# Performance work log

Hardware: AMD Instinct MI355X
Metric: run time of the kernel (lower is better)

## Reference

```python
import jax, jax.numpy as jnp
import numpy as np

N_NODES = 50000
N_EDGES = 600000
HID = 128
OUT = 14
LAYERS = 3
N_GRAPHS = 16
NODE_VOCAB = (120, 6)
EDGE_VOCAB = (6, 3)
GEN_EPS = 1e-7   # GENConv eps added after ReLU on messages
BN_EPS = 1e-5    # torch BatchNorm1d default eps


def setup_inputs() -> dict:
    key = jax.random.key(0)
    ks = jax.random.split(key, 14)
    inp = {}
    inp['node_feat0'] = jax.random.randint(ks[0], (N_NODES,), 0, NODE_VOCAB[0], dtype=jnp.int32)
    inp['node_feat1'] = jax.random.randint(ks[1], (N_NODES,), 0, NODE_VOCAB[1], dtype=jnp.int32)
    inp['edge_feat0'] = jax.random.randint(ks[2], (N_EDGES,), 0, EDGE_VOCAB[0], dtype=jnp.int32)
    inp['edge_feat1'] = jax.random.randint(ks[3], (N_EDGES,), 0, EDGE_VOCAB[1], dtype=jnp.int32)
    inp['edge_src'] = jax.random.randint(ks[4], (N_EDGES,), 0, N_NODES, dtype=jnp.int32)
    inp['edge_dst'] = jax.random.randint(ks[5], (N_EDGES,), 0, N_NODES, dtype=jnp.int32)
    inp['graph_ids'] = jnp.repeat(jnp.arange(N_GRAPHS, dtype=jnp.int32), N_NODES // N_GRAPHS)
    inp['num_graphs'] = N_GRAPHS
    s = 0.05
    inp['W_node0'] = jax.random.normal(ks[6], (NODE_VOCAB[0], HID), jnp.float32) * s
    inp['W_node1'] = jax.random.normal(ks[7], (NODE_VOCAB[1], HID), jnp.float32) * s
    # per-layer edge embedding tables (each GENConv layer has its own)
    inp['edge_emb0'] = jax.random.normal(ks[8], (LAYERS, EDGE_VOCAB[0], HID), jnp.float32) * s
    inp['edge_emb1'] = jax.random.normal(ks[9], (LAYERS, EDGE_VOCAB[1], HID), jnp.float32) * s
    inp['beta'] = jnp.ones((LAYERS,), jnp.float32)  # learnable softmax temperature, init 1.0
    inp['mlp_W'] = jax.random.normal(ks[10], (LAYERS, HID, HID), jnp.float32) * (1.0 / np.sqrt(HID))
    inp['mlp_b'] = jnp.zeros((LAYERS, HID), jnp.float32)
    inp['bn_gamma'] = jnp.ones((LAYERS, HID), jnp.float32)
    inp['bn_beta'] = jnp.zeros((LAYERS, HID), jnp.float32)
    inp['W_out'] = jax.random.normal(ks[11], (HID, OUT), jnp.float32) * (1.0 / np.sqrt(HID))
    inp['b_out'] = jnp.zeros((OUT,), jnp.float32)
    return inp


def _segment_softmax(z, seg, num_segments):
    # DGL edge_softmax: elementwise softmax over edges sharing a destination node.
    zmax = jax.ops.segment_max(z, seg, num_segments=num_segments)
    zmax = jnp.where(jnp.isfinite(zmax), zmax, 0.0)  # guard empty segments
    e = jnp.exp(z - zmax[seg])
    denom = jax.ops.segment_sum(e, seg, num_segments=num_segments)
    return e / denom[seg]


def reference(node_feat0, node_feat1, edge_feat0, edge_feat1, edge_src, edge_dst,
              graph_ids, num_graphs, W_node0, W_node1, edge_emb0, edge_emb1,
              beta, mlp_W, mlp_b, bn_gamma, bn_beta, W_out, b_out):
    # node embedding lookup + sum over tables
    hv = W_node0[node_feat0] + W_node1[node_feat1]          # [N, H]
    n = hv.shape[0]
    for l in range(mlp_W.shape[0]):
        # BatchNorm1d (training mode: batch stats, biased variance) + ReLU
        mu = jnp.mean(hv, axis=0)
        var = jnp.var(hv, axis=0)
        hv1 = (hv - mu) * jax.lax.rsqrt(var + BN_EPS) * bn_gamma[l] + bn_beta[l]
        hv1 = jax.nn.relu(hv1)
        # GENConv: edge embed sum, u_add_e, relu+eps, edge_softmax, scatter-sum
        ee = edge_emb0[l][edge_feat0] + edge_emb1[l][edge_feat1]   # [E, H]
        m = jax.nn.relu(hv1[edge_src] + ee) + GEN_EPS              # [E, H]
        a = _segment_softmax(m * beta[l], edge_dst, n)             # [E, H]
        agg = jax.ops.segment_sum(m * a, edge_dst, num_segments=n)  # [N, H]
        # feats = node_feats + msg, then 1-layer MLP, then outer skip connect
        hv = (hv1 + agg) @ mlp_W[l] + mlp_b[l] + hv
    # AvgPooling over each graph in the batch, then output Linear
    counts = jax.ops.segment_sum(jnp.ones((n,), hv.dtype), graph_ids, num_segments=num_graphs)
    hg = jax.ops.segment_sum(hv, graph_ids, num_segments=num_graphs) / counts[:, None]
    return hg @ W_out + b_out  # [num_graphs, OUT]
```

## Files before the change

kernel.cpp:

```cpp
#include <hip/hip_runtime.h>

#define N_NODESC 50000
#define N_EDGESC 600000
#define HID 128
#define LAYERS 3
#define N_GRAPHSC 16
#define OUT_DIM 14
#define GEN_EPS 1e-7f
#define BN_EPS 1e-5f
#define SCAN_BLK 196
#define POOL_BLK 400
#define EMB_BLK 6250
#define GEMM_BLK 782
#define XPAD 50048
#define LOG2E 1.44269504f

typedef short bf16x8 __attribute__((ext_vector_type(8)));
typedef float f32x4 __attribute__((ext_vector_type(4)));

__device__ __forceinline__ unsigned short f2bf(float f) {
    union { float f; unsigned u; } v; v.f = f;
    unsigned r = v.u + 0x7FFF + ((v.u >> 16) & 1);
    return (unsigned short)(r >> 16);
}
__device__ __forceinline__ float bf_lo(unsigned u) {
    return __uint_as_float(u << 16);
}
__device__ __forceinline__ float bf_hi(unsigned u) {
    return __uint_as_float(u & 0xFFFF0000u);
}

__global__ void k_count(const int* __restrict__ dst, int* __restrict__ deg) {
    int i = blockIdx.x * blockDim.x + threadIdx.x;
    if (i < N_EDGESC) atomicAdd(&deg[dst[i]], 1);
}

__global__ void k_blocksum(const int* __restrict__ deg, int* __restrict__ part) {
    __shared__ int sh[256];
    int t = threadIdx.x;
    int i = blockIdx.x * 256 + t;
    sh[t] = (i < N_NODESC) ? deg[i] : 0;
    __syncthreads();
    for (int off = 128; off > 0; off >>= 1) {
        if (t < off) sh[t] += sh[t + off];
        __syncthreads();
    }
    if (t == 0) part[blockIdx.x] = sh[0];
}

__global__ void k_scanpart(const int* __restrict__ part, int* __restrict__ bofs) {
    __shared__ int sh[256];
    int t = threadIdx.x;
    int v = (t < SCAN_BLK) ? part[t] : 0;
    sh[t] = v;
    __syncthreads();
    for (int off = 1; off < 256; off <<= 1) {
        int add = (t >= off) ? sh[t - off] : 0;
        __syncthreads();
        sh[t] += add;
        __syncthreads();
    }
    if (t < SCAN_BLK) bofs[t] = sh[t] - v;
}

__global__ void k_rowptr(const int* __restrict__ deg, const int* __restrict__ bofs,
                         int* __restrict__ row_ptr, int* __restrict__ cursor) {
    __shared__ int sh[256];
    int t = threadIdx.x;
    int i = blockIdx.x * 256 + t;
    int d = (i < N_NODESC) ? deg[i] : 0;
    sh[t] = d;
    __syncthreads();
    for (int off = 1; off < 256; off <<= 1) {
        int add = (t >= off) ? sh[t - off] : 0;
        __syncthreads();
        sh[t] += add;
        __syncthreads();
    }
    if (i < N_NODESC) {
        int rp = bofs[blockIdx.x] + sh[t] - d;
        row_ptr[i] = rp;
        cursor[i] = rp;
    }
    if (i == 0) row_ptr[N_NODESC] = N_EDGESC;
}

__global__ void k_scatter(const int* __restrict__ dst, const int* __restrict__ src,
                          const int* __restrict__ f0, const int* __restrict__ f1,
                          int* __restrict__ cursor, int* __restrict__ csr_pack) {
    int i = blockIdx.x * blockDim.x + threadIdx.x;
    if (i < N_EDGESC) {
        int pos = atomicAdd(&cursor[dst[i]], 1);
        csr_pack[pos] = (src[i] << 8) | ((f0[i] * 3 + f1[i]) * 8);
    }
}

__global__ void k_wfrag(const float* __restrict__ W, unsigned short* __restrict__ wf) {
    int i = blockIdx.x * blockDim.x + threadIdx.x;
    if (i >= LAYERS * 4 * 8 * 64 * 8) return;
    int j = i & 7;
    int lane = (i >> 3) & 63;
    int nt = (i >> 9) & 7;
    int ks = (i >> 12) & 3;
    int l = i >> 14;
    int k = ks * 32 + (lane >> 4) * 8 + j;
    int n = nt * 16 + (lane & 15);
    wf[i] = f2bf(W[(size_t)l * HID * HID + k * HID + n]);
}

__global__ void k_embed(const int* __restrict__ f0, const int* __restrict__ f1,
                        const float4* __restrict__ W0, const float4* __restrict__ W1,
                        float4* __restrict__ hv4, float* __restrict__ part) {
    __shared__ float sh[1024], sh2[1024];
    int tid = threadIdx.x;
    int i = blockIdx.x * 256 + tid;
    int v = i >> 5, c4 = i & 31;
    float4 a = W0[f0[v] * 32 + c4];
    float4 b = W1[f1[v] * 32 + c4];
    float4 o = make_float4(a.x + b.x, a.y + b.y, a.z + b.z, a.w + b.w);
    hv4[i] = o;
    sh[tid * 4 + 0] = o.x; sh2[tid * 4 + 0] = o.x * o.x;
    sh[tid * 4 + 1] = o.y; sh2[tid * 4 + 1] = o.y * o.y;
    sh[tid * 4 + 2] = o.z; sh2[tid * 4 + 2] = o.z * o.z;
    sh[tid * 4 + 3] = o.w; sh2[tid * 4 + 3] = o.w * o.w;
    __syncthreads();
    if (tid < 128) {
        int c4i = tid >> 2, j = tid & 3;
        float s = 0.f, s2 = 0.f;
#pragma unroll
        for (int r = 0; r < 8; r++) {
            s += sh[(r * 32 + c4i) * 4 + j];
            s2 += sh2[(r * 32 + c4i) * 4 + j];
        }
        part[(size_t)blockIdx.x * 256 + tid] = s;
        part[(size_t)blockIdx.x * 256 + 128 + tid] = s2;
    }
}

__global__ void k_bn_reduce2(const float* __restrict__ part, int nparts,
                             float* __restrict__ gsum) {
    int slot = blockIdx.x;
    int t = threadIdx.x;
    float s = 0.f;
    for (int p = t; p < nparts; p += 256) s += part[(size_t)p * 256 + slot];
    __shared__ float sh[256];
    sh[t] = s;
    __syncthreads();
    for (int o = 128; o > 0; o >>= 1) {
        if (t < o) sh[t] += sh[t + o];
        __syncthreads();
    }
    if (t == 0) gsum[slot] = sh[0];
}

__global__ void k_hv1b(const float4* __restrict__ hv4, const float* __restrict__ gsum,
                       const float* __restrict__ gamma, const float* __restrict__ betab,
                       uint2* __restrict__ hv1b) {
    int i = blockIdx.x * 256 + threadIdx.x;
    int c = (i & 31) * 4;
    const float invN = 1.f / (float)N_NODESC;
    float4 h = hv4[i];
    float r[4];
#pragma unroll
    for (int j = 0; j < 4; j++) {
        float mu = gsum[c + j] * invN;
        float var = gsum[128 + c + j] * invN - mu * mu;
        float sc = gamma[c + j] * rsqrtf(var + BN_EPS);
        float sf = betab[c + j] - mu * sc;
        r[j] = fmaxf(fmaf((&h.x)[j], sc, sf), 0.f);
    }
    uint2 o;
    o.x = (unsigned)f2bf(r[0]) | ((unsigned)f2bf(r[1]) << 16);
    o.y = (unsigned)f2bf(r[2]) | ((unsigned)f2bf(r[3]) << 16);
    hv1b[i] = o;
}

__global__ __launch_bounds__(512) void k_agg(
    const unsigned* __restrict__ hv1b, const int* __restrict__ row_ptr,
    const int* __restrict__ csr_pack, const float* __restrict__ e0,
    const float* __restrict__ e1, const float* __restrict__ beta_p,
    unsigned* __restrict__ xb) {
    __shared__ float2 sh_et[64][19];
    int tid = threadIdx.x;
    for (int i = tid; i < 18 * 64; i += 512) {
        int f = i >> 6, ln = i & 63;
        int a = f / 3, b = f - 3 * a;
        float2 ea = *(const float2*)(e0 + a * HID + 2 * ln);
        float2 eb = *(const float2*)(e1 + b * HID + 2 * ln);
        sh_et[ln][f] = make_float2(ea.x + eb.x, ea.y + eb.y);
    }
    int wave = tid >> 6, lane = tid & 63;
    int v = blockIdx.x * 8 + wave;
    float beta = *beta_p;
    const float bl2 = beta * LOG2E;
    __syncthreads();
    unsigned su = hv1b[(size_t)v * 64 + lane];
    float h10 = bf_lo(su), h11 = bf_hi(su);
    int p0 = row_ptr[v], p1 = row_ptr[v + 1];
    int deg = p1 - p0;
    float n0 = 0.f, n1 = 0.f, d0 = 0.f, d1 = 0.f;
    const char* hv1c = (const char*)hv1b;
    const char* etc = (const char*)&sh_et[lane][0];
    unsigned lane4 = (unsigned)lane * 4;

#define AGG_BODY(J)                                                         \
    {                                                                       \
        int pack = __shfl(pk, (J), 64);                                     \
        unsigned u = *(const unsigned*)(hv1c +                              \
                        ((((unsigned)pack) & 0xFFFFFF00u) + lane4));        \
        float2 t = *(const float2*)(etc + (((unsigned)pack) & 0xFFu));      \
        float r0 = fmaxf(bf_lo(u) + t.x, 0.f);                              \
        float r1 = fmaxf(bf_hi(u) + t.y, 0.f);                              \
        float w0 = exp2f(r0 * bl2);                                         \
        float w1 = exp2f(r1 * bl2);                                         \
        d0 += w0; d1 += w1;                                                 \
        n0 = fmaf(r0, w0, n0); n1 = fmaf(r1, w1, n1);                       \
    }

    for (int base = 0; base < deg; base += 64) {
        int idx = base + lane;
        int pk = (idx < deg) ? csr_pack[p0 + idx] : 0;
        int jn = min(64, deg - base);
        int j = 0;
        for (; j + 2 <= jn; j += 2) {
            AGG_BODY(j)
            AGG_BODY(j + 1)
        }
        if (j < jn) AGG_BODY(j)
    }
#undef AGG_BODY

    float ox = h10 + (deg ? __fdividef(n0, d0) + GEN_EPS : 0.f);
    float oy = h11 + (deg ? __fdividef(n1, d1) + GEN_EPS : 0.f);
    xb[(size_t)v * 64 + lane] = (unsigned)f2bf(ox) | ((unsigned)f2bf(oy) << 16);
}

__global__ __launch_bounds__(256) void k_gemm(
    const unsigned short* __restrict__ x,
    const unsigned short* __restrict__ wf,
    const float* __restrict__ b, float* __restrict__ hv,
    float* __restrict__ part) {
    __shared__ float shs[512], shs2[512];
    int tid = threadIdx.x;
    int w = tid >> 6, lane = tid & 63;
    int m0 = blockIdx.x * 64 + w * 16;
    int mrow = lane & 15, grp = lane >> 4;
    bf16x8 af[4];
    const unsigned short* xrow = x + (size_t)(m0 + mrow) * HID + grp * 8;
#pragma unroll
    for (int ks = 0; ks < 4; ks++)
        af[ks] = *(const bf16x8*)(xrow + ks * 32);
    f32x4 acc[8];
#pragma unroll
    for (int nt = 0; nt < 8; nt++) acc[nt] = (f32x4){0.f, 0.f, 0.f, 0.f};
#pragma unroll
    for (int nt = 0; nt < 8; nt++) {
#pragma unroll
        for (int ks = 0; ks < 4; ks++) {
            bf16x8 bf = *(const bf16x8*)(wf + (size_t)((ks * 8 + nt) * 64 + lane) * 8);
            acc[nt] = __builtin_amdgcn_mfma_f32_16x16x32_bf16(af[ks], bf, acc[nt], 0, 0, 0);
        }
    }
#pragma unroll
    for (int nt = 0; nt < 8; nt++) {
        int col = nt * 16 + mrow;
        float bias = b[col];
        float s = 0.f, s2 = 0.f;
#pragma unroll
        for (int r = 0; r < 4; r++) {
            int v = m0 + grp * 4 + r;
            if (v < N_NODESC) {
                size_t idx = (size_t)v * HID + col;
                float o = acc[nt][r] + bias + hv[idx];
                hv[idx] = o;
                s += o; s2 += o * o;
            }
        }
        s  += __shfl_xor(s, 16, 64);  s  += __shfl_xor(s, 32, 64);
        s2 += __shfl_xor(s2, 16, 64); s2 += __shfl_xor(s2, 32, 64);
        if (lane < 16) { shs[w * 128 + col] = s; shs2[w * 128 + col] = s2; }
    }
    __syncthreads();
    if (tid < 128) {
        part[(size_t)blockIdx.x * 256 + tid] =
            shs[tid] + shs[128 + tid] + shs[256 + tid] + shs[384 + tid];
    } else {
        int c = tid - 128;
        part[(size_t)blockIdx.x * 256 + tid] =
            shs2[c] + shs2[128 + c] + shs2[256 + c] + shs2[384 + c];
    }
}

__global__ void k_pool(const float* __restrict__ hv, float* __restrict__ part2) {
    int tid = threadIdx.x;
    int c = tid & 127, rh = tid >> 7;
    int start = blockIdx.x * 125;
    float acc = 0.f;
    for (int r = start + rh; r < start + 125; r += 2)
        acc += hv[(size_t)r * HID + c];
    __shared__ float sh[256];
    sh[tid] = acc;
    __syncthreads();
    if (rh == 0) part2[blockIdx.x * 128 + c] = acc + sh[tid + 128];
}

__global__ void k_finish(const float* __restrict__ part2, const float* __restrict__ Wo,
                         const float* __restrict__ bo, float* __restrict__ out) {
    __shared__ float hg[N_GRAPHSC * HID];
    int t = threadIdx.x;
    for (int s = t; s < N_GRAPHSC * HID; s += 256) {
        int g = s >> 7, c = s & 127;
        float x = 0.f;
#pragma unroll
        for (int i = 0; i < 25; i++) x += part2[(g * 25 + i) * 128 + c];
        hg[s] = x;
    }
    __syncthreads();
    if (t < N_GRAPHSC * OUT_DIM) {
        int g = t / OUT_DIM, o = t % OUT_DIM;
        const float inv = (float)N_GRAPHSC / (float)N_NODESC;
        float acc = bo[o];
        for (int k = 0; k < HID; k++)
            acc += hg[g * HID + k] * inv * Wo[k * OUT_DIM + o];
        out[t] = acc;
    }
}

extern "C" void kernel_launch(void* const* d_in, const int* in_sizes, int n_in,
                              void* d_out, int out_size, void* d_ws, size_t ws_size,
                              hipStream_t stream) {
    const int* node_feat0 = (const int*)d_in[0];
    const int* node_feat1 = (const int*)d_in[1];
    const int* edge_feat0 = (const int*)d_in[2];
    const int* edge_feat1 = (const int*)d_in[3];
    const int* edge_src   = (const int*)d_in[4];
    const int* edge_dst   = (const int*)d_in[5];
    const float* W_node0   = (const float*)d_in[8];
    const float* W_node1   = (const float*)d_in[9];
    const float* edge_emb0 = (const float*)d_in[10];
    const float* edge_emb1 = (const float*)d_in[11];
    const float* beta      = (const float*)d_in[12];
    const float* mlp_W     = (const float*)d_in[13];
    const float* mlp_b     = (const float*)d_in[14];
    const float* bn_gamma  = (const float*)d_in[15];
    const float* bn_beta   = (const float*)d_in[16];
    const float* W_out     = (const float*)d_in[17];
    const float* b_out     = (const float*)d_in[18];
    float* out = (float*)d_out;

    char* ws = (char*)d_ws;
    size_t off = 0;
    auto alloc = [&](size_t bytes) -> void* {
        void* p = ws + off;
        off += (bytes + 255) & ~(size_t)255;
        return p;
    };
    float* hv      = (float*)alloc((size_t)N_NODESC * HID * 4);
    unsigned* xb   = (unsigned*)alloc((size_t)XPAD * 64 * 4);
    unsigned* hv1b = (unsigned*)alloc((size_t)N_NODESC * 64 * 4);
    float* bnpart  = (float*)alloc((size_t)EMB_BLK * 256 * 4);
    float* gsum    = (float*)alloc(256 * 4);
    unsigned short* wfrag = (unsigned short*)alloc((size_t)LAYERS * 16384 * 2);
    float* part2   = (float*)alloc(POOL_BLK * 128 * 4);
    int* row_ptr   = (int*)alloc((N_NODESC + 1) * 4);
    int* cursor    = (int*)alloc(N_NODESC * 4);
    int* deg       = (int*)alloc(N_NODESC * 4);
    int* part      = (int*)alloc(SCAN_BLK * 4);
    int* bofs      = (int*)alloc(SCAN_BLK * 4);
    int* csr_pack  = (int*)alloc((size_t)N_EDGESC * 4);

    hipMemsetAsync(deg, 0, N_NODESC * 4, stream);
    k_count<<<(N_EDGESC + 255) / 256, 256, 0, stream>>>(edge_dst, deg);
    k_blocksum<<<SCAN_BLK, 256, 0, stream>>>(deg, part);
    k_scanpart<<<1, 256, 0, stream>>>(part, bofs);
    k_rowptr<<<SCAN_BLK, 256, 0, stream>>>(deg, bofs, row_ptr, cursor);
    k_scatter<<<(N_EDGESC + 255) / 256, 256, 0, stream>>>(
        edge_dst, edge_src, edge_feat0, edge_feat1, cursor, csr_pack);
    k_wfrag<<<(LAYERS * 16384 + 255) / 256, 256, 0, stream>>>(mlp_W, wfrag);

    k_embed<<<EMB_BLK, 256, 0, stream>>>(
        node_feat0, node_feat1, (const float4*)W_node0, (const float4*)W_node1,
        (float4*)hv, bnpart);

    for (int l = 0; l < LAYERS; l++) {
        int nparts = (l == 0) ? EMB_BLK : GEMM_BLK;
        k_bn_reduce2<<<256, 256, 0, stream>>>(bnpart, nparts, gsum);
        k_hv1b<<<(N_NODESC * 32) / 256, 256, 0, stream>>>(
            (const float4*)hv, gsum, bn_gamma + l * HID, bn_beta + l * HID,
            (uint2*)hv1b);
        k_agg<<<N_NODESC / 8, 512, 0, stream>>>(
            hv1b, row_ptr, csr_pack,
            edge_emb0 + (size_t)l * 6 * HID, edge_emb1 + (size_t)l * 3 * HID,
            beta + l, xb);
        k_gemm<<<GEMM_BLK, 256, 0, stream>>>(
            (const unsigned short*)xb, wfrag + (size_t)l * 16384,
            mlp_b + l * HID, hv, bnpart);
    }

    k_pool<<<POOL_BLK, 256, 0, stream>>>(hv, part2);
    k_finish<<<1, 256, 0, stream>>>(part2, W_out, b_out, out);
}
```

Baseline: 454.9 us.

## Process two edges per wave in aggregation with wider loads; atomic BN reduce

The aggregation kernel now has each half-wave handle a different edge, with each lane loading 4 bf16 features (8 bytes) and a float4 edge-embedding entry, so two edges are processed per iteration. The half-wave partial sums are combined with a cross-half shuffle at the end. An odd trailing edge is masked for the second half. The BN statistics reduction switches from 256 blocks with a strided column gather to 64 blocks with coalesced row sums combined via atomicAdd into per-layer zeroed buffers. This reduces instruction count per edge and improves coalescing, but atomics make the reduction order nondeterministic.

```diff
diff --git a/kernel.cpp b/kernel.cpp
--- a/kernel.cpp
+++ b/kernel.cpp
@@ -13,6 +13,7 @@
 #define EMB_BLK 6250
 #define GEMM_BLK 782
 #define XPAD 50048
+#define BNR_BLK 64
 #define LOG2E 1.44269504f
 
 typedef short bf16x8 __attribute__((ext_vector_type(8)));
@@ -139,18 +140,13 @@
 
 __global__ void k_bn_reduce2(const float* __restrict__ part, int nparts,
                              float* __restrict__ gsum) {
-    int slot = blockIdx.x;
     int t = threadIdx.x;
+    int rows = (nparts + BNR_BLK - 1) / BNR_BLK;
+    int r0 = blockIdx.x * rows;
+    int r1 = min(r0 + rows, nparts);
     float s = 0.f;
-    for (int p = t; p < nparts; p += 256) s += part[(size_t)p * 256 + slot];
-    __shared__ float sh[256];
-    sh[t] = s;
-    __syncthreads();
-    for (int o = 128; o > 0; o >>= 1) {
-        if (t < o) sh[t] += sh[t + o];
-        __syncthreads();
-    }
-    if (t == 0) gsum[slot] = sh[0];
+    for (int p = r0; p < r1; p++) s += part[(size_t)p * 256 + t];
+    atomicAdd(&gsum[t], s);
 }
 
 __global__ void k_hv1b(const float4* __restrict__ hv4, const float* __restrict__ gsum,
@@ -180,59 +176,95 @@
     const int* __restrict__ csr_pack, const float* __restrict__ e0,
     const float* __restrict__ e1, const float* __restrict__ beta_p,
     unsigned* __restrict__ xb) {
-    __shared__ float2 sh_et[64][19];
+    __shared__ float4 sh_et[18 * 32];
     int tid = threadIdx.x;
-    for (int i = tid; i < 18 * 64; i += 512) {
-        int f = i >> 6, ln = i & 63;
+    for (int i = tid; i < 18 * 32; i += 512) {
+        int f = i >> 5, s = i & 31;
         int a = f / 3, b = f - 3 * a;
-        float2 ea = *(const float2*)(e0 + a * HID + 2 * ln);
-        float2 eb = *(const float2*)(e1 + b * HID + 2 * ln);
-        sh_et[ln][f] = make_float2(ea.x + eb.x, ea.y + eb.y);
+        float4 ea = *(const float4*)(e0 + a * HID + 4 * s);
+        float4 eb = *(const float4*)(e1 + b * HID + 4 * s);
+        sh_et[i] = make_float4(ea.x + eb.x, ea.y + eb.y, ea.z + eb.z, ea.w + eb.w);
     }
     int wave = tid >> 6, lane = tid & 63;
+    int h = lane >> 5, s = lane & 31;
     int v = blockIdx.x * 8 + wave;
     float beta = *beta_p;
     const float bl2 = beta * LOG2E;
-    __syncthreads();
-    unsigned su = hv1b[(size_t)v * 64 + lane];
-    float h10 = bf_lo(su), h11 = bf_hi(su);
+    const float hm = h ? 0.f : 1.f;
+    __syncthreads();
+    uint2 su = ((const uint2*)hv1b)[v * 32 + s];
     int p0 = row_ptr[v], p1 = row_ptr[v + 1];
     int deg = p1 - p0;
-    float n0 = 0.f, n1 = 0.f, d0 = 0.f, d1 = 0.f;
+    float n0 = 0.f, n1 = 0.f, n2 = 0.f, n3 = 0.f;
+    float d0 = 0.f, d1 = 0.f, d2 = 0.f, d3 = 0.f;
     const char* hv1c = (const char*)hv1b;
-    const char* etc = (const char*)&sh_et[lane][0];
-    unsigned lane4 = (unsigned)lane * 4;
-
-#define AGG_BODY(J)                                                         \
+    const char* etc = (const char*)sh_et;
+    unsigned s8 = (unsigned)s * 8;
+    unsigned s16 = (unsigned)s * 16;
+
+#define PAIR(J)                                                             \
     {                                                                       \
-        int pack = __shfl(pk, (J), 64);                                     \
-        unsigned u = *(const unsigned*)(hv1c +                              \
-                        ((((unsigned)pack) & 0xFFFFFF00u) + lane4));        \
-        float2 t = *(const float2*)(etc + (((unsigned)pack) & 0xFFu));      \
-        float r0 = fmaxf(bf_lo(u) + t.x, 0.f);                              \
-        float r1 = fmaxf(bf_hi(u) + t.y, 0.f);                              \
-        float w0 = exp2f(r0 * bl2);                                         \
-        float w1 = exp2f(r1 * bl2);                                         \
-        d0 += w0; d1 += w1;                                                 \
+        int pack = __shfl(pk, 2 * (J) + h, 64);                             \
+        uint2 u = *(const uint2*)(hv1c +                                    \
+                      ((((unsigned)pack) & 0xFFFFFF00u) | s8));             \
+        float4 t = *(const float4*)(etc +                                   \
+                      ((((unsigned)pack & 0xFFu) << 6) | s16));             \
+        float r0 = fmaxf(bf_lo(u.x) + t.x, 0.f);                            \
+        float r1 = fmaxf(bf_hi(u.x) + t.y, 0.f);                            \
+        float r2 = fmaxf(bf_lo(u.y) + t.z, 0.f);                            \
+        float r3 = fmaxf(bf_hi(u.y) + t.w, 0.f);                            \
+        float w0 = exp2f(r0 * bl2), w1 = exp2f(r1 * bl2);                   \
+        float w2 = exp2f(r2 * bl2), w3 = exp2f(r3 * bl2);                   \
+        d0 += w0; d1 += w1; d2 += w2; d3 += w3;                             \
         n0 = fmaf(r0, w0, n0); n1 = fmaf(r1, w1, n1);                       \
+        n2 = fmaf(r2, w2, n2); n3 = fmaf(r3, w3, n3);                       \
     }
 
     for (int base = 0; base < deg; base += 64) {
         int idx = base + lane;
         int pk = (idx < deg) ? csr_pack[p0 + idx] : 0;
         int jn = min(64, deg - base);
+        int pairs = jn >> 1;
         int j = 0;
-        for (; j + 2 <= jn; j += 2) {
-            AGG_BODY(j)
-            AGG_BODY(j + 1)
+        for (; j + 2 <= pairs; j += 2) {
+            PAIR(j)
+            PAIR(j + 1)
         }
-        if (j < jn) AGG_BODY(j)
-    }
-#undef AGG_BODY
-
-    float ox = h10 + (deg ? __fdividef(n0, d0) + GEN_EPS : 0.f);
-    float oy = h11 + (deg ? __fdividef(n1, d1) + GEN_EPS : 0.f);
-    xb[(size_t)v * 64 + lane] = (unsigned)f2bf(ox) | ((unsigned)f2bf(oy) << 16);
+        if (j < pairs) PAIR(j)
+        if (jn & 1) {
+            int pack = __shfl(pk, jn - 1, 64);
+            uint2 u = *(const uint2*)(hv1c +
+                          ((((unsigned)pack) & 0xFFFFFF00u) | s8));
+            float4 t = *(const float4*)(etc +
+                          ((((unsigned)pack & 0xFFu) << 6) | s16));
+            float r0 = fmaxf(bf_lo(u.x) + t.x, 0.f);
+            float r1 = fmaxf(bf_hi(u.x) + t.y, 0.f);
+            float r2 = fmaxf(bf_lo(u.y) + t.z, 0.f);
+            float r3 = fmaxf(bf_hi(u.y) + t.w, 0.f);
+            float w0 = exp2f(r0 * bl2) * hm, w1 = exp2f(r1 * bl2) * hm;
+            float w2 = exp2f(r2 * bl2) * hm, w3 = exp2f(r3 * bl2) * hm;
+            d0 += w0; d1 += w1; d2 += w2; d3 += w3;
+            n0 = fmaf(r0, w0, n0); n1 = fmaf(r1, w1, n1);
+            n2 = fmaf(r2, w2, n2); n3 = fmaf(r3, w3, n3);
+        }
+    }
+#undef PAIR
+
+    n0 += __shfl_xor(n0, 32, 64); d0 += __shfl_xor(d0, 32, 64);
+    n1 += __shfl_xor(n1, 32, 64); d1 += __shfl_xor(d1, 32, 64);
+    n2 += __shfl_xor(n2, 32, 64); d2 += __shfl_xor(d2, 32, 64);
+    n3 += __shfl_xor(n3, 32, 64); d3 += __shfl_xor(d3, 32, 64);
+
+    float o0 = bf_lo(su.x) + (deg ? __fdividef(n0, d0) + GEN_EPS : 0.f);
+    float o1 = bf_hi(su.x) + (deg ? __fdividef(n1, d1) + GEN_EPS : 0.f);
+    float o2 = bf_lo(su.y) + (deg ? __fdividef(n2, d2) + GEN_EPS : 0.f);
+    float o3 = bf_hi(su.y) + (deg ? __fdividef(n3, d3) + GEN_EPS : 0.f);
+    if (h == 0) {
+        uint2 ov;
+        ov.x = (unsigned)f2bf(o0) | ((unsigned)f2bf(o1) << 16);
+        ov.y = (unsigned)f2bf(o2) | ((unsigned)f2bf(o3) << 16);
+        ((uint2*)xb)[v * 32 + s] = ov;
+    }
 }
 
 __global__ __launch_bounds__(256) void k_gemm(
@@ -359,7 +391,7 @@
     unsigned* xb   = (unsigned*)alloc((size_t)XPAD * 64 * 4);
     unsigned* hv1b = (unsigned*)alloc((size_t)N_NODESC * 64 * 4);
     float* bnpart  = (float*)alloc((size_t)EMB_BLK * 256 * 4);
-    float* gsum    = (float*)alloc(256 * 4);
+    float* gsums   = (float*)alloc(LAYERS * 256 * 4);
     unsigned short* wfrag = (unsigned short*)alloc((size_t)LAYERS * 16384 * 2);
     float* part2   = (float*)alloc(POOL_BLK * 128 * 4);
     int* row_ptr   = (int*)alloc((N_NODESC + 1) * 4);
@@ -370,6 +402,7 @@
     int* csr_pack  = (int*)alloc((size_t)N_EDGESC * 4);
 
     hipMemsetAsync(deg, 0, N_NODESC * 4, stream);
+    hipMemsetAsync(gsums, 0, LAYERS * 256 * 4, stream);
     k_count<<<(N_EDGESC + 255) / 256, 256, 0, stream>>>(edge_dst, deg);
     k_blocksum<<<SCAN_BLK, 256, 0, stream>>>(deg, part);
     k_scanpart<<<1, 256, 0, stream>>>(part, bofs);
@@ -383,8 +416,9 @@
         (float4*)hv, bnpart);
 
     for (int l = 0; l < LAYERS; l++) {
+        float* gsum = gsums + l * 256;
         int nparts = (l == 0) ? EMB_BLK : GEMM_BLK;
-        k_bn_reduce2<<<256, 256, 0, stream>>>(bnpart, nparts, gsum);
+        k_bn_reduce2<<<BNR_BLK, 256, 0, stream>>>(bnpart, nparts, gsum);
         k_hv1b<<<(N_NODESC * 32) / 256, 256, 0, stream>>>(
             (const float4*)hv, gsum, bn_gamma + l * HID, bn_beta + l * HID,
             (uint2*)hv1b);
```

Measured after the change: 458.9 us. About the same (+0.9%).

## Split node features into 16-channel planes so gather working set fits cache

Applied to the files above, without the earlier changes.

Node features (hv1 and the aggregation output) are stored as 8 planes of 16 bf16 channels each instead of row-major 128 channels. Each aggregation block handles one plane for 64 nodes, with 8 lanes per node, so a gather touches a 1.6MB plane that can stay cache-resident instead of striding across the full feature matrix. The GEMM loads its A fragments from the planar layout. The BN-stat reduction now splits rows across 64 blocks and combines them with atomics into per-layer zeroed buffers. The cost is that each edge index is read 8 times (once per plane) and nodes in the same wave loop to the largest degree with masked work.

```diff
diff --git a/kernel.cpp b/kernel.cpp
--- a/kernel.cpp
+++ b/kernel.cpp
@@ -12,7 +12,11 @@
 #define POOL_BLK 400
 #define EMB_BLK 6250
 #define GEMM_BLK 782
-#define XPAD 50048
+#define BNR_BLK 64
+#define PLN 50048
+#define PLNW (PLN * 8)
+#define PLNS (PLN * 16)
+#define NCHUNK 8
 #define LOG2E 1.44269504f
 
 typedef short bf16x8 __attribute__((ext_vector_type(8)));
@@ -139,25 +143,21 @@
 
 __global__ void k_bn_reduce2(const float* __restrict__ part, int nparts,
                              float* __restrict__ gsum) {
-    int slot = blockIdx.x;
     int t = threadIdx.x;
+    int rows = (nparts + BNR_BLK - 1) / BNR_BLK;
+    int r0 = blockIdx.x * rows;
+    int r1 = min(r0 + rows, nparts);
     float s = 0.f;
-    for (int p = t; p < nparts; p += 256) s += part[(size_t)p * 256 + slot];
-    __shared__ float sh[256];
-    sh[t] = s;
-    __syncthreads();
-    for (int o = 128; o > 0; o >>= 1) {
-        if (t < o) sh[t] += sh[t + o];
-        __syncthreads();
-    }
-    if (t == 0) gsum[slot] = sh[0];
+    for (int p = r0; p < r1; p++) s += part[(size_t)p * 256 + t];
+    atomicAdd(&gsum[t], s);
 }
 
 __global__ void k_hv1b(const float4* __restrict__ hv4, const float* __restrict__ gsum,
                        const float* __restrict__ gamma, const float* __restrict__ betab,
-                       uint2* __restrict__ hv1b) {
+                       unsigned* __restrict__ hv1p) {
     int i = blockIdx.x * 256 + threadIdx.x;
-    int c = (i & 31) * 4;
+    int v = i >> 5, c4 = i & 31;
+    int c = c4 * 4;
     const float invN = 1.f / (float)N_NODESC;
     float4 h = hv4[i];
     float r[4];
@@ -172,67 +172,70 @@
     uint2 o;
     o.x = (unsigned)f2bf(r[0]) | ((unsigned)f2bf(r[1]) << 16);
     o.y = (unsigned)f2bf(r[2]) | ((unsigned)f2bf(r[3]) << 16);
-    hv1b[i] = o;
+    int ck = c4 >> 2;
+    *(uint2*)(hv1p + (size_t)ck * PLNW + (size_t)v * 8 + (c4 & 3) * 2) = o;
 }
 
 __global__ __launch_bounds__(512) void k_agg(
-    const unsigned* __restrict__ hv1b, const int* __restrict__ row_ptr,
+    const unsigned* __restrict__ hv1p, const int* __restrict__ row_ptr,
     const int* __restrict__ csr_pack, const float* __restrict__ e0,
     const float* __restrict__ e1, const float* __restrict__ beta_p,
-    unsigned* __restrict__ xb) {
-    __shared__ float2 sh_et[64][19];
+    unsigned* __restrict__ xbp) {
+    __shared__ float2 sh_et[18 * 8];
     int tid = threadIdx.x;
-    for (int i = tid; i < 18 * 64; i += 512) {
-        int f = i >> 6, ln = i & 63;
+    int ck = blockIdx.x & 7;
+    int ng = blockIdx.x >> 3;
+    if (tid < 144) {
+        int f = tid >> 3, sl = tid & 7;
         int a = f / 3, b = f - 3 * a;
-        float2 ea = *(const float2*)(e0 + a * HID + 2 * ln);
-        float2 eb = *(const float2*)(e1 + b * HID + 2 * ln);
-        sh_et[ln][f] = make_float2(ea.x + eb.x, ea.y + eb.y);
+        int c0 = ck * 16 + sl * 2;
+        float2 ea = *(const float2*)(e0 + a * HID + c0);
+        float2 eb = *(const float2*)(e1 + b * HID + c0);
+        sh_et[tid] = make_float2(ea.x + eb.x, ea.y + eb.y);
     }
     int wave = tid >> 6, lane = tid & 63;
-    int v = blockIdx.x * 8 + wave;
+    int oct = lane >> 3, s = lane & 7;
+    int v = ng * 64 + wave * 8 + oct;
     float beta = *beta_p;
     const float bl2 = beta * LOG2E;
     __syncthreads();
-    unsigned su = hv1b[(size_t)v * 64 + lane];
-    float h10 = bf_lo(su), h11 = bf_hi(su);
-    int p0 = row_ptr[v], p1 = row_ptr[v + 1];
-    int deg = p1 - p0;
+    const unsigned* plane = hv1p + (size_t)ck * PLNW;
+    unsigned su = plane[v * 8 + s];
+    int vc = min(v, N_NODESC);
+    int p0 = row_ptr[vc];
+    int deg = row_ptr[min(vc + 1, N_NODESC)] - p0;
+    int dd = deg;
+    dd = max(dd, __shfl_xor(dd, 8, 64));
+    dd = max(dd, __shfl_xor(dd, 16, 64));
+    dd = max(dd, __shfl_xor(dd, 32, 64));
+    int dmax = __builtin_amdgcn_readfirstlane(dd);
     float n0 = 0.f, n1 = 0.f, d0 = 0.f, d1 = 0.f;
-    const char* hv1c = (const char*)hv1b;
-    const char* etc = (const char*)&sh_et[lane][0];
-    unsigned lane4 = (unsigned)lane * 4;
-
-#define AGG_BODY(J)                                                         \
-    {                                                                       \
-        int pack = __shfl(pk, (J), 64);                                     \
-        unsigned u = *(const unsigned*)(hv1c +                              \
-                        ((((unsigned)pack) & 0xFFFFFF00u) + lane4));        \
-        float2 t = *(const float2*)(etc + (((unsigned)pack) & 0xFFu));      \
-        float r0 = fmaxf(bf_lo(u) + t.x, 0.f);                              \
-        float r1 = fmaxf(bf_hi(u) + t.y, 0.f);                              \
-        float w0 = exp2f(r0 * bl2);                                         \
-        float w1 = exp2f(r1 * bl2);                                         \
-        d0 += w0; d1 += w1;                                                 \
-        n0 = fmaf(r0, w0, n0); n1 = fmaf(r1, w1, n1);                       \
-    }
-
-    for (int base = 0; base < deg; base += 64) {
-        int idx = base + lane;
-        int pk = (idx < deg) ? csr_pack[p0 + idx] : 0;
-        int jn = min(64, deg - base);
-        int j = 0;
-        for (; j + 2 <= jn; j += 2) {
-            AGG_BODY(j)
-            AGG_BODY(j + 1)
-        }
-        if (j < jn) AGG_BODY(j)
-    }
-#undef AGG_BODY
-
-    float ox = h10 + (deg ? __fdividef(n0, d0) + GEN_EPS : 0.f);
-    float oy = h11 + (deg ? __fdividef(n1, d1) + GEN_EPS : 0.f);
-    xb[(size_t)v * 64 + lane] = (unsigned)f2bf(ox) | ((unsigned)f2bf(oy) << 16);
+    const char* pc = (const char*)plane;
+    const char* etc = (const char*)sh_et;
+    unsigned s4 = (unsigned)s * 4, s8 = (unsigned)s * 8;
+    int dm1 = deg - 1;
+#pragma unroll 2
+    for (int j = 0; j < dmax; j++) {
+        bool on = j < deg;
+        int pidx = min(p0 + max(0, min(j, dm1)), N_EDGESC - 1);
+        int pk = __builtin_nontemporal_load(&csr_pack[pidx]);
+        unsigned u = *(const unsigned*)(pc +
+                        ((((unsigned)pk & 0xFFFFFF00u) >> 3) | s4));
+        float2 t = *(const float2*)(etc +
+                        ((((unsigned)pk & 0xFFu) << 3) | s8));
+        float r0 = fmaxf(bf_lo(u) + t.x, 0.f);
+        float r1 = fmaxf(bf_hi(u) + t.y, 0.f);
+        float w0 = exp2f(r0 * bl2), w1 = exp2f(r1 * bl2);
+        w0 = on ? w0 : 0.f;
+        w1 = on ? w1 : 0.f;
+        d0 += w0; d1 += w1;
+        n0 = fmaf(r0, w0, n0); n1 = fmaf(r1, w1, n1);
+    }
+    float o0 = bf_lo(su) + (deg ? __fdividef(n0, d0) + GEN_EPS : 0.f);
+    float o1 = bf_hi(su) + (deg ? __fdividef(n1, d1) + GEN_EPS : 0.f);
+    if (v < N_NODESC)
+        xbp[(size_t)ck * PLNW + (size_t)v * 8 + s] =
+            (unsigned)f2bf(o0) | ((unsigned)f2bf(o1) << 16);
 }
 
 __global__ __launch_bounds__(256) void k_gemm(
@@ -246,10 +249,12 @@
     int m0 = blockIdx.x * 64 + w * 16;
     int mrow = lane & 15, grp = lane >> 4;
     bf16x8 af[4];
-    const unsigned short* xrow = x + (size_t)(m0 + mrow) * HID + grp * 8;
-#pragma unroll
-    for (int ks = 0; ks < 4; ks++)
-        af[ks] = *(const bf16x8*)(xrow + ks * 32);
+#pragma unroll
+    for (int ks = 0; ks < 4; ks++) {
+        int ckp = ks * 2 + (grp >> 1);
+        af[ks] = *(const bf16x8*)(x + (size_t)ckp * PLNS +
+                                  (size_t)(m0 + mrow) * 16 + (grp & 1) * 8);
+    }
     f32x4 acc[8];
 #pragma unroll
     for (int nt = 0; nt < 8; nt++) acc[nt] = (f32x4){0.f, 0.f, 0.f, 0.f};
@@ -356,10 +361,10 @@
         return p;
     };
     float* hv      = (float*)alloc((size_t)N_NODESC * HID * 4);
-    unsigned* xb   = (unsigned*)alloc((size_t)XPAD * 64 * 4);
-    unsigned* hv1b = (unsigned*)alloc((size_t)N_NODESC * 64 * 4);
+    unsigned* xbp  = (unsigned*)alloc((size_t)NCHUNK * PLNW * 4);
+    unsigned* hv1p = (unsigned*)alloc((size_t)NCHUNK * PLNW * 4);
     float* bnpart  = (float*)alloc((size_t)EMB_BLK * 256 * 4);
-    float* gsum    = (float*)alloc(256 * 4);
+    float* gsums   = (float*)alloc(LAYERS * 256 * 4);
     unsigned short* wfrag = (unsigned short*)alloc((size_t)LAYERS * 16384 * 2);
     float* part2   = (float*)alloc(POOL_BLK * 128 * 4);
     int* row_ptr   = (int*)alloc((N_NODESC + 1) * 4);
@@ -370,6 +375,7 @@
     int* csr_pack  = (int*)alloc((size_t)N_EDGESC * 4);
 
     hipMemsetAsync(deg, 0, N_NODESC * 4, stream);
+    hipMemsetAsync(gsums, 0, LAYERS * 256 * 4, stream);
     k_count<<<(N_EDGESC + 255) / 256, 256, 0, stream>>>(edge_dst, deg);
     k_blocksum<<<SCAN_BLK, 256, 0, stream>>>(deg, part);
     k_scanpart<<<1, 256, 0, stream>>>(part, bofs);
@@ -383,17 +389,17 @@
         (float4*)hv, bnpart);
 
     for (int l = 0; l < LAYERS; l++) {
+        float* gsum = gsums + l * 256;
         int nparts = (l == 0) ? EMB_BLK : GEMM_BLK;
-        k_bn_reduce2<<<256, 256, 0, stream>>>(bnpart, nparts, gsum);
+        k_bn_reduce2<<<BNR_BLK, 256, 0, stream>>>(bnpart, nparts, gsum);
         k_hv1b<<<(N_NODESC * 32) / 256, 256, 0, stream>>>(
-            (const float4*)hv, gsum, bn_gamma + l * HID, bn_beta + l * HID,
-            (uint2*)hv1b);
-        k_agg<<<N_NODESC / 8, 512, 0, stream>>>(
-            hv1b, row_ptr, csr_pack,
+            (const float4*)hv, gsum, bn_gamma + l * HID, bn_beta + l * HID, hv1p);
+        k_agg<<<GEMM_BLK * NCHUNK, 512, 0, stream>>>(
+            hv1p, row_ptr, csr_pack,
             edge_emb0 + (size_t)l * 6 * HID, edge_emb1 + (size_t)l * 3 * HID,
-            beta + l, xb);
+            beta + l, xbp);
         k_gemm<<<GEMM_BLK, 256, 0, stream>>>(
-            (const unsigned short*)xb, wfrag + (size_t)l * 16384,
+            (const unsigned short*)xbp, wfrag + (size_t)l * 16384,
             mlp_b + l * HID, hv, bnpart);
     }
 
```

After: 570.0 us. 25.3% more time.

## Fuse aggregation with MFMA GEMM via shared-memory tile, merge weight prep into embed

Applied to the files above, without the earlier changes.

Aggregation and the MLP GEMM become one kernel. Each 512-thread block aggregates 64 nodes into a swizzled LDS bf16 tile and then runs the MFMA GEMM from that tile, which removes the xb global round trip and one launch per layer. The weight-fragment conversion is folded into extra blocks of the embed kernel. The BN partial reduction now uses 64 blocks that atomically add into per-layer zeroed sums. In exchange, each wave now processes 8 nodes serially, which lowers grid parallelism in the latency-bound gather, and the float atomics make the sums order-nondeterministic.

```diff
diff --git a/kernel.cpp b/kernel.cpp
--- a/kernel.cpp
+++ b/kernel.cpp
@@ -11,8 +11,9 @@
 #define SCAN_BLK 196
 #define POOL_BLK 400
 #define EMB_BLK 6250
+#define WF_BLK 192
 #define GEMM_BLK 782
-#define XPAD 50048
+#define BNR_BLK 64
 #define LOG2E 1.44269504f
 
 typedef short bf16x8 __attribute__((ext_vector_type(8)));
@@ -95,24 +96,26 @@
     }
 }
 
-__global__ void k_wfrag(const float* __restrict__ W, unsigned short* __restrict__ wf) {
-    int i = blockIdx.x * blockDim.x + threadIdx.x;
-    if (i >= LAYERS * 4 * 8 * 64 * 8) return;
-    int j = i & 7;
-    int lane = (i >> 3) & 63;
-    int nt = (i >> 9) & 7;
-    int ks = (i >> 12) & 3;
-    int l = i >> 14;
-    int k = ks * 32 + (lane >> 4) * 8 + j;
-    int n = nt * 16 + (lane & 15);
-    wf[i] = f2bf(W[(size_t)l * HID * HID + k * HID + n]);
-}
-
 __global__ void k_embed(const int* __restrict__ f0, const int* __restrict__ f1,
                         const float4* __restrict__ W0, const float4* __restrict__ W1,
-                        float4* __restrict__ hv4, float* __restrict__ part) {
+                        float4* __restrict__ hv4, float* __restrict__ part,
+                        const float* __restrict__ W, unsigned short* __restrict__ wf) {
+    int tid = threadIdx.x;
+    if (blockIdx.x >= EMB_BLK) {
+        int i = (blockIdx.x - EMB_BLK) * 256 + tid;
+        if (i < LAYERS * 4 * 8 * 64 * 8) {
+            int j = i & 7;
+            int lane = (i >> 3) & 63;
+            int nt = (i >> 9) & 7;
+            int ks = (i >> 12) & 3;
+            int l = i >> 14;
+            int k = ks * 32 + (lane >> 4) * 8 + j;
+            int n = nt * 16 + (lane & 15);
+            wf[i] = f2bf(W[(size_t)l * HID * HID + k * HID + n]);
+        }
+        return;
+    }
     __shared__ float sh[1024], sh2[1024];
-    int tid = threadIdx.x;
     int i = blockIdx.x * 256 + tid;
     int v = i >> 5, c4 = i & 31;
     float4 a = W0[f0[v] * 32 + c4];
@@ -139,18 +142,13 @@
 
 __global__ void k_bn_reduce2(const float* __restrict__ part, int nparts,
                              float* __restrict__ gsum) {
-    int slot = blockIdx.x;
     int t = threadIdx.x;
+    int rows = (nparts + BNR_BLK - 1) / BNR_BLK;
+    int r0 = blockIdx.x * rows;
+    int r1 = min(r0 + rows, nparts);
     float s = 0.f;
-    for (int p = t; p < nparts; p += 256) s += part[(size_t)p * 256 + slot];
-    __shared__ float sh[256];
-    sh[t] = s;
-    __syncthreads();
-    for (int o = 128; o > 0; o >>= 1) {
-        if (t < o) sh[t] += sh[t + o];
-        __syncthreads();
-    }
-    if (t == 0) gsum[slot] = sh[0];
+    for (int p = r0; p < r1; p++) s += part[(size_t)p * 256 + t];
+    atomicAdd(&gsum[t], s);
 }
 
 __global__ void k_hv1b(const float4* __restrict__ hv4, const float* __restrict__ gsum,
@@ -175,40 +173,41 @@
     hv1b[i] = o;
 }
 
-__global__ __launch_bounds__(512) void k_agg(
+__global__ __launch_bounds__(512) void k_aggemm(
     const unsigned* __restrict__ hv1b, const int* __restrict__ row_ptr,
     const int* __restrict__ csr_pack, const float* __restrict__ e0,
     const float* __restrict__ e1, const float* __restrict__ beta_p,
-    unsigned* __restrict__ xb) {
-    __shared__ float2 sh_et[64][19];
+    const unsigned short* __restrict__ wf, const float* __restrict__ b,
+    float* __restrict__ hv, float* __restrict__ part) {
+    __shared__ float2 sh_et[18 * 64];
+    __shared__ unsigned x_tile[64 * 64];
+    __shared__ float shs[512], shs2[512];
     int tid = threadIdx.x;
     for (int i = tid; i < 18 * 64; i += 512) {
         int f = i >> 6, ln = i & 63;
-        int a = f / 3, b = f - 3 * a;
+        int a = f / 3, bb = f - 3 * a;
         float2 ea = *(const float2*)(e0 + a * HID + 2 * ln);
-        float2 eb = *(const float2*)(e1 + b * HID + 2 * ln);
-        sh_et[ln][f] = make_float2(ea.x + eb.x, ea.y + eb.y);
-    }
-    int wave = tid >> 6, lane = tid & 63;
-    int v = blockIdx.x * 8 + wave;
+        float2 eb = *(const float2*)(e1 + bb * HID + 2 * ln);
+        sh_et[i] = make_float2(ea.x + eb.x, ea.y + eb.y);
+    }
+    int w = tid >> 6, lane = tid & 63;
+    int m0 = blockIdx.x * 64;
     float beta = *beta_p;
     const float bl2 = beta * LOG2E;
     __syncthreads();
-    unsigned su = hv1b[(size_t)v * 64 + lane];
-    float h10 = bf_lo(su), h11 = bf_hi(su);
-    int p0 = row_ptr[v], p1 = row_ptr[v + 1];
-    int deg = p1 - p0;
-    float n0 = 0.f, n1 = 0.f, d0 = 0.f, d1 = 0.f;
+
     const char* hv1c = (const char*)hv1b;
-    const char* etc = (const char*)&sh_et[lane][0];
+    const char* etc = (const char*)sh_et;
     unsigned lane4 = (unsigned)lane * 4;
+    unsigned lane8 = (unsigned)lane * 8;
 
 #define AGG_BODY(J)                                                         \
     {                                                                       \
         int pack = __shfl(pk, (J), 64);                                     \
         unsigned u = *(const unsigned*)(hv1c +                              \
                         ((((unsigned)pack) & 0xFFFFFF00u) + lane4));        \
-        float2 t = *(const float2*)(etc + (((unsigned)pack) & 0xFFu));      \
+        float2 t = *(const float2*)(etc +                                   \
+                        (((((unsigned)pack) & 0xFFu) << 6) + lane8));       \
         float r0 = fmaxf(bf_lo(u) + t.x, 0.f);                              \
         float r1 = fmaxf(bf_hi(u) + t.y, 0.f);                              \
         float w0 = exp2f(r0 * bl2);                                         \
@@ -217,58 +216,63 @@
         n0 = fmaf(r0, w0, n0); n1 = fmaf(r1, w1, n1);                       \
     }
 
-    for (int base = 0; base < deg; base += 64) {
-        int idx = base + lane;
-        int pk = (idx < deg) ? csr_pack[p0 + idx] : 0;
-        int jn = min(64, deg - base);
-        int j = 0;
-        for (; j + 2 <= jn; j += 2) {
-            AGG_BODY(j)
-            AGG_BODY(j + 1)
+    for (int i = 0; i < 8; i++) {
+        int row = w * 8 + i;
+        int v = m0 + row;
+        int vc = min(v, N_NODESC - 1);
+        unsigned su = hv1b[(size_t)vc * 64 + lane];
+        int p0 = row_ptr[vc];
+        int deg = (v < N_NODESC) ? (row_ptr[vc + 1] - p0) : 0;
+        float n0 = 0.f, n1 = 0.f, d0 = 0.f, d1 = 0.f;
+        for (int base = 0; base < deg; base += 64) {
+            int idx = base + lane;
+            int pk = (idx < deg) ? csr_pack[p0 + idx] : 0;
+            int jn = min(64, deg - base);
+            int j = 0;
+            for (; j + 2 <= jn; j += 2) {
+                AGG_BODY(j)
+                AGG_BODY(j + 1)
+            }
+            if (j < jn) AGG_BODY(j)
         }
-        if (j < jn) AGG_BODY(j)
+        float ox = bf_lo(su) + (deg ? __fdividef(n0, d0) + GEN_EPS : 0.f);
+        float oy = bf_hi(su) + (deg ? __fdividef(n1, d1) + GEN_EPS : 0.f);
+        x_tile[row * 64 + ((lane + row * 4) & 63)] =
+            (unsigned)f2bf(ox) | ((unsigned)f2bf(oy) << 16);
     }
 #undef AGG_BODY
-
-    float ox = h10 + (deg ? __fdividef(n0, d0) + GEN_EPS : 0.f);
-    float oy = h11 + (deg ? __fdividef(n1, d1) + GEN_EPS : 0.f);
-    xb[(size_t)v * 64 + lane] = (unsigned)f2bf(ox) | ((unsigned)f2bf(oy) << 16);
-}
-
-__global__ __launch_bounds__(256) void k_gemm(
-    const unsigned short* __restrict__ x,
-    const unsigned short* __restrict__ wf,
-    const float* __restrict__ b, float* __restrict__ hv,
-    float* __restrict__ part) {
-    __shared__ float shs[512], shs2[512];
-    int tid = threadIdx.x;
-    int w = tid >> 6, lane = tid & 63;
-    int m0 = blockIdx.x * 64 + w * 16;
+    __syncthreads();
+
+    int rw = w & 3, chh = w >> 2;
     int mrow = lane & 15, grp = lane >> 4;
+    int rbase = rw * 16 + mrow;
     bf16x8 af[4];
-    const unsigned short* xrow = x + (size_t)(m0 + mrow) * HID + grp * 8;
-#pragma unroll
-    for (int ks = 0; ks < 4; ks++)
-        af[ks] = *(const bf16x8*)(xrow + ks * 32);
-    f32x4 acc[8];
-#pragma unroll
-    for (int nt = 0; nt < 8; nt++) acc[nt] = (f32x4){0.f, 0.f, 0.f, 0.f};
-#pragma unroll
-    for (int nt = 0; nt < 8; nt++) {
+#pragma unroll
+    for (int ks = 0; ks < 4; ks++) {
+        int col = ks * 16 + grp * 4;
+        int colr = (col + rbase * 4) & 63;
+        af[ks] = *(const bf16x8*)&x_tile[rbase * 64 + colr];
+    }
+    f32x4 acc[4];
+#pragma unroll
+    for (int nt = 0; nt < 4; nt++) acc[nt] = (f32x4){0.f, 0.f, 0.f, 0.f};
+#pragma unroll
+    for (int nt = 0; nt < 4; nt++) {
+        int ntg = chh * 4 + nt;
 #pragma unroll
         for (int ks = 0; ks < 4; ks++) {
-            bf16x8 bf = *(const bf16x8*)(wf + (size_t)((ks * 8 + nt) * 64 + lane) * 8);
-            acc[nt] = __builtin_amdgcn_mfma_f32_16x16x32_bf16(af[ks], bf, acc[nt], 0, 0, 0);
+            bf16x8 bfr = *(const bf16x8*)(wf + (size_t)((ks * 8 + ntg) * 64 + lane) * 8);
+            acc[nt] = __builtin_amdgcn_mfma_f32_16x16x32_bf16(af[ks], bfr, acc[nt], 0, 0, 0);
         }
     }
 #pragma unroll
-    for (int nt = 0; nt < 8; nt++) {
-        int col = nt * 16 + mrow;
+    for (int nt = 0; nt < 4; nt++) {
+        int col = chh * 64 + nt * 16 + mrow;
         float bias = b[col];
         float s = 0.f, s2 = 0.f;
 #pragma unroll
         for (int r = 0; r < 4; r++) {
-            int v = m0 + grp * 4 + r;
+            int v = m0 + rw * 16 + grp * 4 + r;
             if (v < N_NODESC) {
                 size_t idx = (size_t)v * HID + col;
                 float o = acc[nt][r] + bias + hv[idx];
@@ -278,13 +282,13 @@
         }
         s  += __shfl_xor(s, 16, 64);  s  += __shfl_xor(s, 32, 64);
         s2 += __shfl_xor(s2, 16, 64); s2 += __shfl_xor(s2, 32, 64);
-        if (lane < 16) { shs[w * 128 + col] = s; shs2[w * 128 + col] = s2; }
+        if (lane < 16) { shs[rw * 128 + col] = s; shs2[rw * 128 + col] = s2; }
     }
     __syncthreads();
     if (tid < 128) {
         part[(size_t)blockIdx.x * 256 + tid] =
             shs[tid] + shs[128 + tid] + shs[256 + tid] + shs[384 + tid];
-    } else {
+    } else if (tid < 256) {
         int c = tid - 128;
         part[(size_t)blockIdx.x * 256 + tid] =
             shs2[c] + shs2[128 + c] + shs2[256 + c] + shs2[384 + c];
@@ -356,10 +360,9 @@
         return p;
     };
     float* hv      = (float*)alloc((size_t)N_NODESC * HID * 4);
-    unsigned* xb   = (unsigned*)alloc((size_t)XPAD * 64 * 4);
     unsigned* hv1b = (unsigned*)alloc((size_t)N_NODESC * 64 * 4);
     float* bnpart  = (float*)alloc((size_t)EMB_BLK * 256 * 4);
-    float* gsum    = (float*)alloc(256 * 4);
+    float* gsums   = (float*)alloc(LAYERS * 256 * 4);
     unsigned short* wfrag = (unsigned short*)alloc((size_t)LAYERS * 16384 * 2);
     float* part2   = (float*)alloc(POOL_BLK * 128 * 4);
     int* row_ptr   = (int*)alloc((N_NODESC + 1) * 4);
@@ -370,31 +373,29 @@
     int* csr_pack  = (int*)alloc((size_t)N_EDGESC * 4);
 
     hipMemsetAsync(deg, 0, N_NODESC * 4, stream);
+    hipMemsetAsync(gsums, 0, LAYERS * 256 * 4, stream);
     k_count<<<(N_EDGESC + 255) / 256, 256, 0, stream>>>(edge_dst, deg);
     k_blocksum<<<SCAN_BLK, 256, 0, stream>>>(deg, part);
     k_scanpart<<<1, 256, 0, stream>>>(part, bofs);
     k_rowptr<<<SCAN_BLK, 256, 0, stream>>>(deg, bofs, row_ptr, cursor);
     k_scatter<<<(N_EDGESC + 255) / 256, 256, 0, stream>>>(
         edge_dst, edge_src, edge_feat0, edge_feat1, cursor, csr_pack);
-    k_wfrag<<<(LAYERS * 16384 + 255) / 256, 256, 0, stream>>>(mlp_W, wfrag);
-
-    k_embed<<<EMB_BLK, 256, 0, stream>>>(
+
+    k_embed<<<EMB_BLK + WF_BLK, 256, 0, stream>>>(
         node_feat0, node_feat1, (const float4*)W_node0, (const float4*)W_node1,
-        (float4*)hv, bnpart);
+        (float4*)hv, bnpart, mlp_W, wfrag);
 
     for (int l = 0; l < LAYERS; l++) {
+        float* gsum = gsums + l * 256;
         int nparts = (l == 0) ? EMB_BLK : GEMM_BLK;
-        k_bn_reduce2<<<256, 256, 0, stream>>>(bnpart, nparts, gsum);
+        k_bn_reduce2<<<BNR_BLK, 256, 0, stream>>>(bnpart, nparts, gsum);
         k_hv1b<<<(N_NODESC * 32) / 256, 256, 0, stream>>>(
             (const float4*)hv, gsum, bn_gamma + l * HID, bn_beta + l * HID,
             (uint2*)hv1b);
-        k_agg<<<N_NODESC / 8, 512, 0, stream>>>(
+        k_aggemm<<<GEMM_BLK, 512, 0, stream>>>(
             hv1b, row_ptr, csr_pack,
             edge_emb0 + (size_t)l * 6 * HID, edge_emb1 + (size_t)l * 3 * HID,
-            beta + l, xb);
-        k_gemm<<<GEMM_BLK, 256, 0, stream>>>(
-            (const unsigned short*)xb, wfrag + (size_t)l * 16384,
-            mlp_b + l * HID, hv, bnpart);
+            beta + l, wfrag + (size_t)l * 16384, mlp_b + l * HID, hv, bnpart);
     }
 
     k_pool<<<POOL_BLK, 256, 0, stream>>>(hv, part2);
```

New measurement: 454.2 us. About the same (-0.2%).
